# Kernel tuning notes

Hardware: AMD Instinct MI355X
Metric: run time of the kernel (lower is better)

Reference implementation:

```python
import jax, jax.numpy as jnp
import numpy as np

NUM_HEADS = 8
GROUPS = 32
EPS = 1e-5


def setup_inputs() -> dict:
    key = jax.random.key(0)
    k1, k2, k3 = jax.random.split(key, 3)
    B, C, H, W = 16, 512, 64, 64
    x = jax.random.normal(k1, (B, C, H, W), dtype=jnp.float32)
    scale = C ** -0.5  # keep qkv/proj outputs well-scaled
    return {
        "x": x,
        "norm_w": jnp.ones((C,), jnp.float32),
        "norm_b": jnp.zeros((C,), jnp.float32),
        "qkv_w": jax.random.normal(k2, (3 * C, C), dtype=jnp.float32) * scale,
        "qkv_b": jnp.zeros((3 * C,), jnp.float32),
        "proj_w": jax.random.normal(k3, (C, C), dtype=jnp.float32) * scale,
        "proj_b": jnp.zeros((C,), jnp.float32),
    }


def reference(x, norm_w, norm_b, qkv_w, qkv_b, proj_w, proj_b):
    B, C, H, W = x.shape
    N = H * W
    nh = NUM_HEADS
    hd = C // nh

    # GroupNorm(32, C)
    xg = x.reshape(B, GROUPS, C // GROUPS, N)
    mu = xg.mean(axis=(2, 3), keepdims=True)
    var = xg.var(axis=(2, 3), keepdims=True)
    h = ((xg - mu) * jax.lax.rsqrt(var + EPS)).reshape(B, C, N)
    h = h * norm_w[None, :, None] + norm_b[None, :, None]

    h = h.transpose(0, 2, 1)  # [B, N, C]
    qkv = (h @ qkv_w.T + qkv_b).reshape(B, N, 3, nh, hd)
    q, k, v = qkv[:, :, 0], qkv[:, :, 1], qkv[:, :, 2]  # each [B, N, nh, hd]

    # Faithful to source: attention over the HEAD axis at each position
    attn = jnp.einsum('bnhd,bngd->bnhg', q, k) * (hd ** -0.5)  # [B, N, nh, nh]
    attn = jax.nn.softmax(attn, axis=-1)
    o = jnp.einsum('bnhg,bngd->bnhd', attn, v).reshape(B, N, C)

    o = o @ proj_w.T + proj_b  # [B, N, C]
    return x + o.transpose(0, 2, 1).reshape(B, C, H, W)
```

## Files before the change

### kernel.cpp

```cpp
#include <hip/hip_runtime.h>

typedef __attribute__((ext_vector_type(8))) short short8v;
typedef __attribute__((ext_vector_type(4))) float float4v;
typedef unsigned short ushortT;

__device__ __forceinline__ unsigned short f2bf(float f) {
  union { float f; unsigned u; } a; a.f = f;
  unsigned r = a.u + 0x7fffu + ((a.u >> 16) & 1u);
  return (unsigned short)(r >> 16);
}
__device__ __forceinline__ float2 up2(unsigned u) {
  union { unsigned u; float f; } a, b;
  a.u = u << 16; b.u = u & 0xffff0000u;
  return make_float2(a.f, b.f);
}
__device__ __forceinline__ void gl_lds16(const void* g, void* l) {
  __builtin_amdgcn_global_load_lds(
      (const __attribute__((address_space(1))) void*)g,
      (__attribute__((address_space(3))) void*)l, 16, 0, 0);
}

#define WAITV4 asm volatile("s_waitcnt vmcnt(4)" ::: "memory")
#define WAITV0 asm volatile("s_waitcnt vmcnt(0)" ::: "memory")
#define BAR()  __builtin_amdgcn_s_barrier()
#define MFMA16(d, a, b) d = __builtin_amdgcn_mfma_f32_16x16x32_bf16(a, b, d, 0, 0, 0)

__global__ __launch_bounds__(256) void prep(const float* __restrict__ qkvw,
                                            const float* __restrict__ pw,
                                            const float* __restrict__ x,
                                            ushortT* __restrict__ wq_b,
                                            ushortT* __restrict__ wp_b,
                                            float2* __restrict__ stats) {
  int bid = blockIdx.x, tid = threadIdx.x;
  if (bid < 1024) {
    const float* src = (bid < 768) ? qkvw : pw;
    ushortT* dst     = (bid < 768) ? wq_b : wp_b;
    int base = (bid < 768) ? bid : (bid - 768);
    int i = (base * 256 + tid) * 4;
    float4 v = *(const float4*)(src + i);
    uint2 o;
    o.x = (unsigned)f2bf(v.x) | ((unsigned)f2bf(v.y) << 16);
    o.y = (unsigned)f2bf(v.z) | ((unsigned)f2bf(v.w) << 16);
    *(uint2*)(dst + i) = o;
    return;
  }
  int bg = bid - 1024;
  const float* base = x + (size_t)bg * 65536;
  float s = 0.f, s2 = 0.f;
  for (int i = tid; i < 16384; i += 256) {
    float4 v = *(const float4*)(base + (size_t)i * 4);
    s  += v.x + v.y + v.z + v.w;
    s2 += v.x * v.x + v.y * v.y + v.z * v.z + v.w * v.w;
  }
  #pragma unroll
  for (int off = 32; off > 0; off >>= 1) {
    s  += __shfl_down(s, off);
    s2 += __shfl_down(s2, off);
  }
  __shared__ float red[8];
  int w = tid >> 6, l = tid & 63;
  if (l == 0) { red[w] = s; red[w + 4] = s2; }
  __syncthreads();
  if (tid == 0) {
    float ts = red[0] + red[1] + red[2] + red[3];
    float t2 = red[4] + red[5] + red[6] + red[7];
    float mean = ts * (1.f / 65536.f);
    float var  = t2 * (1.f / 65536.f) - mean * mean;
    stats[bg] = make_float2(mean, rsqrtf(var + 1e-5f));
  }
}

__global__ __launch_bounds__(512) void norm_tr(const float* __restrict__ x,
                                               const float* __restrict__ nw,
                                               const float* __restrict__ nb,
                                               const float2* __restrict__ stats,
                                               ushortT* __restrict__ h) {
  __shared__ float t[64][65];
  int n0 = blockIdx.x * 64, c0 = blockIdx.y * 64, b = blockIdx.z;
  int tx = threadIdx.x, ty = threadIdx.y;
  #pragma unroll
  for (int j = ty; j < 64; j += 8) {
    int c = c0 + j;
    float2 ms = stats[b * 32 + (c >> 4)];
    float v = x[((size_t)b * 512 + c) * 4096 + n0 + tx];
    t[j][tx] = (v - ms.x) * ms.y * nw[c] + nb[c];
  }
  __syncthreads();
  #pragma unroll
  for (int j = ty; j < 64; j += 8) {
    int n = n0 + j;
    h[((size_t)b * 4096 + n) * 512 + c0 + tx] = f2bf(t[tx][j]);
  }
}

__device__ __forceinline__ void core256b(const ushortT* __restrict__ A,
                                         const ushortT* __restrict__ Bm,
                                         ushortT* lds, int m0, int n0,
                                         float4v (&acc)[8][4]) {
  char* ldsb = (char*)lds;
  const int tid = threadIdx.x;
  const int w = tid >> 6, l = tid & 63;
  const int wm = w >> 2, wn = w & 3;

  const int P0b = tid * 16, P1b = 8192 + tid * 16;
  const int r0 = P0b >> 7, r1 = P1b >> 7;
  const int s0 = (P0b & 127) ^ ((r0 & 7) << 4);
  const int s1 = (P1b & 127) ^ ((r1 & 7) << 4);
  const size_t g0 = (size_t)r0 * 512 + (s0 >> 1);
  const size_t g1 = (size_t)r1 * 512 + (s1 >> 1);
  auto stage = [&](const ushortT* mat, int rowbase, int kt, int bufb, int region) {
    const ushortT* gsrc = mat + (size_t)rowbase * 512 + kt * 64;
    char* dbase = ldsb + bufb + region;
    gl_lds16(gsrc + g0, dbase + P0b);
    gl_lds16(gsrc + g1, dbase + P1b);
  };

  const int colb = (l >> 4) * 16;
  const int cs0 = colb ^ ((l & 7) << 4);
  const int cs1 = (64 + colb) ^ ((l & 7) << 4);
  const int arow = wm * 16384 + (l & 15) * 128;
  const int brow = 32768 + wn * 8192 + (l & 15) * 128;

  short8v Af[4][2], Bf[4][2];

  #define RDA4(bb, MH)                                                  \
    { _Pragma("unroll")                                                 \
      for (int mm = 0; mm < 4; ++mm) {                                  \
        const char* p = ldsb + (bb) + arow + ((MH)*4 + mm) * 2048;      \
        Af[mm][0] = *(const short8v*)(p + cs0);                         \
        Af[mm][1] = *(const short8v*)(p + cs1);                         \
      } }
  #define RDB2(bb, N0)                                                  \
    { _Pragma("unroll")                                                 \
      for (int nn = 0; nn < 2; ++nn) {                                  \
        const char* p = ldsb + (bb) + brow + ((N0) + nn) * 2048;        \
        Bf[(N0)+nn][0] = *(const short8v*)(p + cs0);                    \
        Bf[(N0)+nn][1] = *(const short8v*)(p + cs1);                    \
      } }
  #define CLUSTER(MH, NP)                                               \
    { __builtin_amdgcn_s_setprio(1);                                    \
      _Pragma("unroll")                                                 \
      for (int mm = 0; mm < 4; ++mm) {                                  \
        _Pragma("unroll")                                               \
        for (int nn = 0; nn < 2; ++nn) {                                \
          MFMA16(acc[(MH)*4+mm][(NP)*2+nn], Af[mm][0], Bf[(NP)*2+nn][0]); \
          MFMA16(acc[(MH)*4+mm][(NP)*2+nn], Af[mm][1], Bf[(NP)*2+nn][1]); \
        } }                                                             \
      __builtin_amdgcn_s_setprio(0); }

  auto tile = [&](int bb, int t1, int t2, bool s1g, bool s2g, int vw) {
    RDB2(bb, 0); RDA4(bb, 0);
    if (s1g) stage(A, m0 + 128, t1, bb ^ 65536, 16384);
    BAR();
    CLUSTER(0, 0);
    BAR();
    RDB2(bb, 2);
    if (s1g) stage(Bm, n0 + 128, t1, bb ^ 65536, 49152);
    BAR();
    CLUSTER(0, 1);
    BAR();
    RDA4(bb, 1);
    if (s2g) stage(Bm, n0, t2, bb, 32768);
    BAR();
    CLUSTER(1, 1);
    BAR();
    if (s2g) stage(A, m0, t2, bb, 0);
    if (vw == 4)      { WAITV4; }
    else if (vw == 0) { WAITV0; }
    BAR();
    CLUSTER(1, 0);
    BAR();
  };

  stage(A,  m0,       0, 0, 0);
  stage(A,  m0 + 128, 0, 0, 16384);
  stage(Bm, n0,       0, 0, 32768);
  stage(Bm, n0 + 128, 0, 0, 49152);
  stage(Bm, n0,       1, 65536, 32768);
  stage(A,  m0,       1, 65536, 0);
  WAITV4;
  BAR();

  #pragma unroll 1
  for (int tp = 0; tp < 3; ++tp) {
    tile(0,     2 * tp + 1, 2 * tp + 2, true, true, 4);
    tile(65536, 2 * tp + 2, 2 * tp + 3, true, true, 4);
  }
  tile(0,     7, 8, true,  false, 0);
  tile(65536, 8, 9, false, false, -1);
  #undef RDA4
  #undef RDB2
  #undef CLUSTER
}

__device__ __forceinline__ void core128(const ushortT* __restrict__ A,
                                        const ushortT* __restrict__ Bm,
                                        ushortT* lds, int m0, int n0,
                                        float4v (&acc)[4][4]) {
  char* ldsb = (char*)lds;
  const int tid = threadIdx.x;
  const int w = tid >> 6, l = tid & 63;
  const int wm = w >> 1, wn = w & 1;

  const int r0 = tid >> 2, r1 = (256 + tid) >> 2;
  const int s0 = (tid & 3) ^ ((r0 >> 1) & 3);
  const int s1 = (tid & 3) ^ ((r1 >> 1) & 3);
  const size_t gA0 = (size_t)r0 * 512 + s0 * 8;
  const size_t gA1 = (size_t)r1 * 512 + s1 * 8;
  const int d0 = tid * 16, d1 = (256 + tid) * 16;

  const int cs = ((l >> 4) ^ (((l & 15) >> 1) & 3)) * 16;
  const int ab = wm * 4096 + (l & 15) * 64 + cs;
  const int bb = 8192 + wn * 4096 + (l & 15) * 64 + cs;

  const ushortT* pa = A + (size_t)m0 * 512;
  const ushortT* pb = Bm + (size_t)n0 * 512;

  #pragma unroll 1
  for (int kt = 0; kt < 16; ++kt) {
    if (kt) __syncthreads();
    gl_lds16(pa + gA0 + kt * 32, ldsb + d0);
    gl_lds16(pa + gA1 + kt * 32, ldsb + d1);
    gl_lds16(pb + gA0 + kt * 32, ldsb + 8192 + d0);
    gl_lds16(pb + gA1 + kt * 32, ldsb + 8192 + d1);
    __syncthreads();
    short8v Af[4], Bf[4];
    #pragma unroll
    for (int i = 0; i < 4; ++i) {
      Af[i] = *(const short8v*)(ldsb + ab + i * 1024);
      Bf[i] = *(const short8v*)(ldsb + bb + i * 1024);
    }
    #pragma unroll
    for (int mi = 0; mi < 4; ++mi)
      #pragma unroll
      for (int ni = 0; ni < 4; ++ni)
        MFMA16(acc[mi][ni], Af[mi], Bf[ni]);
  }
}

__global__ __launch_bounds__(512, 2) void gemm_qkv(const ushortT* __restrict__ h,
                                                   const ushortT* __restrict__ wq,
                                                   const float* __restrict__ bias,
                                                   ushortT* __restrict__ outq) {
  __shared__ ushortT lds[65536];
  int bid = blockIdx.x;
  int wg = (bid & 7) * 192 + (bid >> 3);
  int m0 = (wg / 6) * 256, n0 = (wg % 6) * 256;
  float4v acc[8][4] = {};
  core256b(h, wq, lds, m0, n0, acc);
  const int tid = threadIdx.x;
  const int w = tid >> 6, l = tid & 63;
  const int wm = w >> 2, wn = w & 3;
  __syncthreads();
  ushortT* es = lds + w * 1280;
  float bb[4];
  #pragma unroll
  for (int fn = 0; fn < 4; ++fn) bb[fn] = bias[n0 + wn * 64 + fn * 16 + (l & 15)];
  int r = l >> 2, g = l & 3;
  #pragma unroll
  for (int fm = 0; fm < 8; ++fm) {
    #pragma unroll
    for (int fn = 0; fn < 4; ++fn)
      #pragma unroll
      for (int j = 0; j < 4; ++j)
        es[((l >> 4) * 4 + j) * 72 + fn * 16 + (l & 15)] = f2bf(acc[fm][fn][j] + bb[fn]);
    uint4 v0 = *(const uint4*)(es + r * 72 + g * 16);
    uint4 v1 = *(const uint4*)(es + r * 72 + g * 16 + 8);
    size_t mrow = (size_t)m0 + wm * 128 + fm * 16 + r;
    uint4* dst = (uint4*)(outq + mrow * 1536 + n0 + wn * 64 + g * 16);
    dst[0] = v0; dst[1] = v1;
  }
}

__global__ __launch_bounds__(256) void attn_k(const ushortT* __restrict__ qkv,
                                              ushortT* __restrict__ o) {
  __shared__ ushortT kv[16 * 1544];
  const int tid = threadIdx.x;
  const int p0 = blockIdx.x * 16;

  #pragma unroll
  for (int j = 0; j < 12; ++j) {
    int c = j * 256 + tid;
    int row = c / 192, col = c % 192;
    gl_lds16(qkv + (size_t)(p0 + row) * 1536 + col * 8,
             (char*)kv + row * 3088 + col * 16);
  }
  __syncthreads();

  const int pos = tid >> 4, h = (tid >> 1) & 7, dh = tid & 1;
  const ushortT* rowp = kv + pos * 1544;

  unsigned qv[16];
  {
    const uint4* qs = (const uint4*)(rowp + h * 64 + dh * 32);
    #pragma unroll
    for (int i = 0; i < 4; ++i) {
      uint4 u = qs[i];
      qv[i*4+0] = u.x; qv[i*4+1] = u.y; qv[i*4+2] = u.z; qv[i*4+3] = u.w;
    }
  }
  float lg[8];
  #pragma unroll
  for (int g = 0; g < 8; ++g) {
    const uint4* ks = (const uint4*)(rowp + 512 + g * 64 + dh * 32);
    float s = 0.f;
    #pragma unroll
    for (int i = 0; i < 4; ++i) {
      uint4 u = ks[i];
      float2 k0 = up2(u.x), k1 = up2(u.y), k2 = up2(u.z), k3 = up2(u.w);
      float2 q0 = up2(qv[i*4+0]), q1 = up2(qv[i*4+1]);
      float2 q2 = up2(qv[i*4+2]), q3 = up2(qv[i*4+3]);
      s += q0.x*k0.x + q0.y*k0.y + q1.x*k1.x + q1.y*k1.y
         + q2.x*k2.x + q2.y*k2.y + q3.x*k3.x + q3.y*k3.y;
    }
    s += __shfl_xor(s, 1);
    lg[g] = s * 0.125f;
  }
  float mx = lg[0];
  #pragma unroll
  for (int g = 1; g < 8; ++g) mx = fmaxf(mx, lg[g]);
  float ssum = 0.f;
  #pragma unroll
  for (int g = 0; g < 8; ++g) { lg[g] = __expf(lg[g] - mx); ssum += lg[g]; }
  float inv = 1.f / ssum;
  #pragma unroll
  for (int g = 0; g < 8; ++g) lg[g] *= inv;

  float oa[32];
  #pragma unroll
  for (int i = 0; i < 32; ++i) oa[i] = 0.f;
  #pragma unroll
  for (int g = 0; g < 8; ++g) {
    const uint4* vs = (const uint4*)(rowp + 1024 + g * 64 + dh * 32);
    float wg = lg[g];
    #pragma unroll
    for (int i = 0; i < 4; ++i) {
      uint4 u = vs[i];
      float2 v0 = up2(u.x), v1 = up2(u.y), v2 = up2(u.z), v3 = up2(u.w);
      oa[i*8+0] += wg*v0.x; oa[i*8+1] += wg*v0.y;
      oa[i*8+2] += wg*v1.x; oa[i*8+3] += wg*v1.y;
      oa[i*8+4] += wg*v2.x; oa[i*8+5] += wg*v2.y;
      oa[i*8+6] += wg*v3.x; oa[i*8+7] += wg*v3.y;
    }
  }
  ushortT* dst = o + (size_t)(p0 + pos) * 512 + h * 64 + dh * 32;
  #pragma unroll
  for (int i = 0; i < 4; ++i) {
    uint4 w_;
    w_.x = (unsigned)f2bf(oa[i*8+0]) | ((unsigned)f2bf(oa[i*8+1]) << 16);
    w_.y = (unsigned)f2bf(oa[i*8+2]) | ((unsigned)f2bf(oa[i*8+3]) << 16);
    w_.z = (unsigned)f2bf(oa[i*8+4]) | ((unsigned)f2bf(oa[i*8+5]) << 16);
    w_.w = (unsigned)f2bf(oa[i*8+6]) | ((unsigned)f2bf(oa[i*8+7]) << 16);
    *(uint4*)(dst + i * 8) = w_;
  }
}

__global__ __launch_bounds__(256) void gemm_proj(const ushortT* __restrict__ o,
                                                 const ushortT* __restrict__ wp,
                                                 const float* __restrict__ bias,
                                                 const float* __restrict__ x,
                                                 float* __restrict__ out) {
  __shared__ ushortT lds[8192];
  int bid = blockIdx.x;
  int wg = (bid & 7) * 256 + (bid >> 3);
  int m0 = (wg >> 2) * 128, n0 = (wg & 3) * 128;
  float4v acc[4][4] = {};
  core128(o, wp, lds, m0, n0, acc);
  const int tid = threadIdx.x;
  const int w = tid >> 6, l = tid & 63;
  const int wm = w >> 1, wn = w & 1;
  __syncthreads();
  float* es = (float*)lds + w * 1024;
  int b = m0 >> 12;
  int c = n0 + wn * 64 + l;
  float bc = bias[c];
  const float* xrow = x + ((size_t)b * 512 + c) * 4096;
  float* orow = out + ((size_t)b * 512 + c) * 4096;
  int nb0 = (m0 & 4095) + wm * 64;
  #pragma unroll
  for (int fm = 0; fm < 4; ++fm) {
    #pragma unroll
    for (int fn = 0; fn < 4; ++fn)
      #pragma unroll
      for (int j = 0; j < 4; ++j)
        es[((l >> 4) * 4 + j) * 64 + fn * 16 + (l & 15)] = acc[fm][fn][j];
    int nb = nb0 + fm * 16;
    #pragma unroll
    for (int q4 = 0; q4 < 4; ++q4) {
      float4 xv = *(const float4*)(xrow + nb + q4 * 4);
      float4 ov;
      ov.x = xv.x + bc + es[(q4 * 4 + 0) * 64 + l];
      ov.y = xv.y + bc + es[(q4 * 4 + 1) * 64 + l];
      ov.z = xv.z + bc + es[(q4 * 4 + 2) * 64 + l];
      ov.w = xv.w + bc + es[(q4 * 4 + 3) * 64 + l];
      *(float4*)(orow + nb + q4 * 4) = ov;
    }
  }
}

extern "C" void kernel_launch(void* const* d_in, const int* in_sizes, int n_in,
                              void* d_out, int out_size, void* d_ws, size_t ws_size,
                              hipStream_t stream) {
  const float* x     = (const float*)d_in[0];
  const float* nw    = (const float*)d_in[1];
  const float* nb    = (const float*)d_in[2];
  const float* qkvw  = (const float*)d_in[3];
  const float* qkvb  = (const float*)d_in[4];
  const float* pw    = (const float*)d_in[5];
  const float* pb    = (const float*)d_in[6];
  float* out = (float*)d_out;
  char* ws = (char*)d_ws;

  const size_t OFF_WQ   = 4096;
  const size_t OFF_WP   = OFF_WQ + 1572864;
  const size_t OFF_H    = OFF_WP + 524288;
  const size_t OFF_QKV  = OFF_H + 67108864;

  float2* stats   = (float2*)ws;
  ushortT* wq_b   = (ushortT*)(ws + OFF_WQ);
  ushortT* wp_b   = (ushortT*)(ws + OFF_WP);
  ushortT* h      = (ushortT*)(ws + OFF_H);
  ushortT* qkv    = (ushortT*)(ws + OFF_QKV);

  prep<<<1536, 256, 0, stream>>>(qkvw, pw, x, wq_b, wp_b, stats);
  norm_tr<<<dim3(64, 8, 16), dim3(64, 8), 0, stream>>>(x, nw, nb, stats, h);
  gemm_qkv<<<1536, 512, 0, stream>>>(h, wq_b, qkvb, qkv);
  attn_k<<<4096, 256, 0, stream>>>(qkv, h);
  gemm_proj<<<2048, 256, 0, stream>>>(h, wp_b, pb, x, out);
}
```

Baseline: 353.4 us.

## Process two M-tiles per QKV GEMM block, prefetching the next tile's first K-slice

The QKV GEMM kernel is inlined and each workgroup now computes two consecutive 256x256 output tiles, so the grid is halved. While the last K-step of the first tile runs, the first K-slice of the second tile is staged into the idle LDS buffer. The epilogue staging area is moved to an LDS region that does not overlap the prefetched data. This aims to hide pipeline fill and epilogue latency between tiles. The cost is more complex control flow, fewer blocks for wave balancing, and more register pressure.

```diff
diff --git a/kernel.cpp b/kernel.cpp
--- a/kernel.cpp
+++ b/kernel.cpp
@@ -93,11 +93,17 @@
   }
 }
 
-__device__ __forceinline__ void core256b(const ushortT* __restrict__ A,
-                                         const ushortT* __restrict__ Bm,
-                                         ushortT* lds, int m0, int n0,
-                                         float4v (&acc)[8][4]) {
+__global__ __launch_bounds__(512, 2) void gemm_qkv(const ushortT* __restrict__ h,
+                                                   const ushortT* __restrict__ wq,
+                                                   const float* __restrict__ bias,
+                                                   ushortT* __restrict__ outq) {
+  __shared__ ushortT lds[65536];
   char* ldsb = (char*)lds;
+  int bid = blockIdx.x;
+  int wg = (bid & 7) * 96 + (bid >> 3);
+  const int m0s = (wg / 6) * 512;
+  const int n0  = (wg % 6) * 256;
+
   const int tid = threadIdx.x;
   const int w = tid >> 6, l = tid & 63;
   const int wm = w >> 2, wn = w & 3;
@@ -121,6 +127,7 @@
   const int arow = wm * 16384 + (l & 15) * 128;
   const int brow = 32768 + wn * 8192 + (l & 15) * 128;
 
+  float4v acc[8][4];
   short8v Af[4][2], Bf[4][2];
 
   #define RDA4(bb, MH)                                                  \
@@ -148,23 +155,23 @@
         } }                                                             \
       __builtin_amdgcn_s_setprio(0); }
 
-  auto tile = [&](int bb, int t1, int t2, bool s1g, bool s2g, int vw) {
+  auto tile = [&](int bb, int t1, int t2, bool s1g, bool s2g, int vw, int mc) {
     RDB2(bb, 0); RDA4(bb, 0);
-    if (s1g) stage(A, m0 + 128, t1, bb ^ 65536, 16384);
+    if (s1g) stage(h, mc + 128, t1, bb ^ 65536, 16384);
     BAR();
     CLUSTER(0, 0);
     BAR();
     RDB2(bb, 2);
-    if (s1g) stage(Bm, n0 + 128, t1, bb ^ 65536, 49152);
+    if (s1g) stage(wq, n0 + 128, t1, bb ^ 65536, 49152);
     BAR();
     CLUSTER(0, 1);
     BAR();
     RDA4(bb, 1);
-    if (s2g) stage(Bm, n0, t2, bb, 32768);
+    if (s2g) stage(wq, n0, t2, bb, 32768);
     BAR();
     CLUSTER(1, 1);
     BAR();
-    if (s2g) stage(A, m0, t2, bb, 0);
+    if (s2g) stage(h, mc, t2, bb, 0);
     if (vw == 4)      { WAITV4; }
     else if (vw == 0) { WAITV0; }
     BAR();
@@ -172,25 +179,168 @@
     BAR();
   };
 
-  stage(A,  m0,       0, 0, 0);
-  stage(A,  m0 + 128, 0, 0, 16384);
-  stage(Bm, n0,       0, 0, 32768);
-  stage(Bm, n0 + 128, 0, 0, 49152);
-  stage(Bm, n0,       1, 65536, 32768);
-  stage(A,  m0,       1, 65536, 0);
-  WAITV4;
-  BAR();
+  auto epilogue = [&](int mc) {
+    ushortT* es = (ushortT*)(ldsb + (w < 6 ? 81920 + w * 2560
+                                           : 114688 + (w - 6) * 2560));
+    float bb4[4];
+    #pragma unroll
+    for (int fn = 0; fn < 4; ++fn)
+      bb4[fn] = bias[n0 + wn * 64 + fn * 16 + (l & 15)];
+    int r = l >> 2, g = l & 3;
+    #pragma unroll
+    for (int fm = 0; fm < 8; ++fm) {
+      #pragma unroll
+      for (int fn = 0; fn < 4; ++fn)
+        #pragma unroll
+        for (int j = 0; j < 4; ++j)
+          es[((l >> 4) * 4 + j) * 72 + fn * 16 + (l & 15)] = f2bf(acc[fm][fn][j] + bb4[fn]);
+      uint4 v0 = *(const uint4*)(es + r * 72 + g * 16);
+      uint4 v1 = *(const uint4*)(es + r * 72 + g * 16 + 8);
+      size_t mrow = (size_t)mc + wm * 128 + fm * 16 + r;
+      uint4* dst = (uint4*)(outq + mrow * 1536 + n0 + wn * 64 + g * 16);
+      dst[0] = v0; dst[1] = v1;
+    }
+  };
 
   #pragma unroll 1
-  for (int tp = 0; tp < 3; ++tp) {
-    tile(0,     2 * tp + 1, 2 * tp + 2, true, true, 4);
-    tile(65536, 2 * tp + 2, 2 * tp + 3, true, true, 4);
-  }
-  tile(0,     7, 8, true,  false, 0);
-  tile(65536, 8, 9, false, false, -1);
+  for (int half = 0; half < 2; ++half) {
+    const int mc = m0s + half * 256;
+    #pragma unroll
+    for (int i = 0; i < 8; ++i)
+      #pragma unroll
+      for (int j = 0; j < 4; ++j)
+        acc[i][j] = (float4v){0.f, 0.f, 0.f, 0.f};
+
+    if (half == 0) {
+      stage(h,  mc,       0, 0, 0);
+      stage(h,  mc + 128, 0, 0, 16384);
+      stage(wq, n0,       0, 0, 32768);
+      stage(wq, n0 + 128, 0, 0, 49152);
+      stage(wq, n0,       1, 65536, 32768);
+      stage(h,  mc,       1, 65536, 0);
+      WAITV4;
+      BAR();
+    } else {
+      stage(wq, n0, 1, 65536, 32768);
+      stage(h,  mc, 1, 65536, 0);
+      BAR();
+    }
+
+    #pragma unroll 1
+    for (int tp = 0; tp < 3; ++tp) {
+      tile(0,     2 * tp + 1, 2 * tp + 2, true, true, 4, mc);
+      tile(65536, 2 * tp + 2, 2 * tp + 3, true, true, 4, mc);
+    }
+    tile(0, 7, 8, true, false, 0, mc);
+
+    if (half == 0) {
+      const int mc2 = mc + 256;
+      RDB2(65536, 0); RDA4(65536, 0);
+      stage(h, mc2, 0, 0, 0);
+      BAR(); CLUSTER(0, 0); BAR();
+      RDB2(65536, 2);
+      stage(h, mc2 + 128, 0, 0, 16384);
+      BAR(); CLUSTER(0, 1); BAR();
+      RDA4(65536, 1);
+      stage(wq, n0, 0, 0, 32768);
+      BAR(); CLUSTER(1, 1); BAR();
+      stage(wq, n0 + 128, 0, 0, 49152);
+      BAR(); CLUSTER(1, 0); BAR();
+    } else {
+      tile(65536, 8, 9, false, false, -1, mc);
+    }
+
+    __syncthreads();
+    epilogue(mc);
+    __syncthreads();
+    if (half == 0) { WAITV0; BAR(); }
+  }
   #undef RDA4
   #undef RDB2
   #undef CLUSTER
+}
+
+__global__ __launch_bounds__(256) void attn_k(const ushortT* __restrict__ qkv,
+                                              ushortT* __restrict__ o) {
+  __shared__ ushortT kv[16 * 1544];
+  const int tid = threadIdx.x;
+  const int p0 = blockIdx.x * 16;
+
+  #pragma unroll
+  for (int j = 0; j < 12; ++j) {
+    int c = j * 256 + tid;
+    int row = c / 192, col = c % 192;
+    gl_lds16(qkv + (size_t)(p0 + row) * 1536 + col * 8,
+             (char*)kv + row * 3088 + col * 16);
+  }
+  __syncthreads();
+
+  const int pos = tid >> 4, h = (tid >> 1) & 7, dh = tid & 1;
+  const ushortT* rowp = kv + pos * 1544;
+
+  unsigned qv[16];
+  {
+    const uint4* qs = (const uint4*)(rowp + h * 64 + dh * 32);
+    #pragma unroll
+    for (int i = 0; i < 4; ++i) {
+      uint4 u = qs[i];
+      qv[i*4+0] = u.x; qv[i*4+1] = u.y; qv[i*4+2] = u.z; qv[i*4+3] = u.w;
+    }
+  }
+  float lg[8];
+  #pragma unroll
+  for (int g = 0; g < 8; ++g) {
+    const uint4* ks = (const uint4*)(rowp + 512 + g * 64 + dh * 32);
+    float s = 0.f;
+    #pragma unroll
+    for (int i = 0; i < 4; ++i) {
+      uint4 u = ks[i];
+      float2 k0 = up2(u.x), k1 = up2(u.y), k2 = up2(u.z), k3 = up2(u.w);
+      float2 q0 = up2(qv[i*4+0]), q1 = up2(qv[i*4+1]);
+      float2 q2 = up2(qv[i*4+2]), q3 = up2(qv[i*4+3]);
+      s += q0.x*k0.x + q0.y*k0.y + q1.x*k1.x + q1.y*k1.y
+         + q2.x*k2.x + q2.y*k2.y + q3.x*k3.x + q3.y*k3.y;
+    }
+    s += __shfl_xor(s, 1);
+    lg[g] = s * 0.125f;
+  }
+  float mx = lg[0];
+  #pragma unroll
+  for (int g = 1; g < 8; ++g) mx = fmaxf(mx, lg[g]);
+  float ssum = 0.f;
+  #pragma unroll
+  for (int g = 0; g < 8; ++g) { lg[g] = __expf(lg[g] - mx); ssum += lg[g]; }
+  float inv = 1.f / ssum;
+  #pragma unroll
+  for (int g = 0; g < 8; ++g) lg[g] *= inv;
+
+  float oa[32];
+  #pragma unroll
+  for (int i = 0; i < 32; ++i) oa[i] = 0.f;
+  #pragma unroll
+  for (int g = 0; g < 8; ++g) {
+    const uint4* vs = (const uint4*)(rowp + 1024 + g * 64 + dh * 32);
+    float wg = lg[g];
+    #pragma unroll
+    for (int i = 0; i < 4; ++i) {
+      uint4 u = vs[i];
+      float2 v0 = up2(u.x), v1 = up2(u.y), v2 = up2(u.z), v3 = up2(u.w);
+      oa[i*8+0] += wg*v0.x; oa[i*8+1] += wg*v0.y;
+      oa[i*8+2] += wg*v1.x; oa[i*8+3] += wg*v1.y;
+      oa[i*8+4] += wg*v2.x; oa[i*8+5] += wg*v2.y;
+      oa[i*8+6] += wg*v3.x; oa[i*8+7] += wg*v3.y;
+    }
+  }
+  ushortT* dst = o + (size_t)(p0 + pos) * 512 + h * 64 + dh * 32;
+  #pragma unroll
+  for (int i = 0; i < 4; ++i) {
+    uint4 w_;
+    w_.x = (unsigned)f2bf(oa[i*8+0]) | ((unsigned)f2bf(oa[i*8+1]) << 16);
+    w_.y = (unsigned)f2bf(oa[i*8+2]) | ((unsigned)f2bf(oa[i*8+3]) << 16);
+    w_.z = (unsigned)f2bf(oa[i*8+4]) | ((unsigned)f2bf(oa[i*8+5]) << 16);
+    w_.w = (unsigned)f2bf(oa[i*8+6]) | ((unsigned)f2bf(oa[i*8+7]) << 16);
+    *(uint4*)(dst + i * 8) = w_;
+  }
 }
 
 __device__ __forceinline__ void core128(const ushortT* __restrict__ A,
@@ -235,123 +385,6 @@
       #pragma unroll
       for (int ni = 0; ni < 4; ++ni)
         MFMA16(acc[mi][ni], Af[mi], Bf[ni]);
-  }
-}
-
-__global__ __launch_bounds__(512, 2) void gemm_qkv(const ushortT* __restrict__ h,
-                                                   const ushortT* __restrict__ wq,
-                                                   const float* __restrict__ bias,
-                                                   ushortT* __restrict__ outq) {
-  __shared__ ushortT lds[65536];
-  int bid = blockIdx.x;
-  int wg = (bid & 7) * 192 + (bid >> 3);
-  int m0 = (wg / 6) * 256, n0 = (wg % 6) * 256;
-  float4v acc[8][4] = {};
-  core256b(h, wq, lds, m0, n0, acc);
-  const int tid = threadIdx.x;
-  const int w = tid >> 6, l = tid & 63;
-  const int wm = w >> 2, wn = w & 3;
-  __syncthreads();
-  ushortT* es = lds + w * 1280;
-  float bb[4];
-  #pragma unroll
-  for (int fn = 0; fn < 4; ++fn) bb[fn] = bias[n0 + wn * 64 + fn * 16 + (l & 15)];
-  int r = l >> 2, g = l & 3;
-  #pragma unroll
-  for (int fm = 0; fm < 8; ++fm) {
-    #pragma unroll
-    for (int fn = 0; fn < 4; ++fn)
-      #pragma unroll
-      for (int j = 0; j < 4; ++j)
-        es[((l >> 4) * 4 + j) * 72 + fn * 16 + (l & 15)] = f2bf(acc[fm][fn][j] + bb[fn]);
-    uint4 v0 = *(const uint4*)(es + r * 72 + g * 16);
-    uint4 v1 = *(const uint4*)(es + r * 72 + g * 16 + 8);
-    size_t mrow = (size_t)m0 + wm * 128 + fm * 16 + r;
-    uint4* dst = (uint4*)(outq + mrow * 1536 + n0 + wn * 64 + g * 16);
-    dst[0] = v0; dst[1] = v1;
-  }
-}
-
-__global__ __launch_bounds__(256) void attn_k(const ushortT* __restrict__ qkv,
-                                              ushortT* __restrict__ o) {
-  __shared__ ushortT kv[16 * 1544];
-  const int tid = threadIdx.x;
-  const int p0 = blockIdx.x * 16;
-
-  #pragma unroll
-  for (int j = 0; j < 12; ++j) {
-    int c = j * 256 + tid;
-    int row = c / 192, col = c % 192;
-    gl_lds16(qkv + (size_t)(p0 + row) * 1536 + col * 8,
-             (char*)kv + row * 3088 + col * 16);
-  }
-  __syncthreads();
-
-  const int pos = tid >> 4, h = (tid >> 1) & 7, dh = tid & 1;
-  const ushortT* rowp = kv + pos * 1544;
-
-  unsigned qv[16];
-  {
-    const uint4* qs = (const uint4*)(rowp + h * 64 + dh * 32);
-    #pragma unroll
-    for (int i = 0; i < 4; ++i) {
-      uint4 u = qs[i];
-      qv[i*4+0] = u.x; qv[i*4+1] = u.y; qv[i*4+2] = u.z; qv[i*4+3] = u.w;
-    }
-  }
-  float lg[8];
-  #pragma unroll
-  for (int g = 0; g < 8; ++g) {
-    const uint4* ks = (const uint4*)(rowp + 512 + g * 64 + dh * 32);
-    float s = 0.f;
-    #pragma unroll
-    for (int i = 0; i < 4; ++i) {
-      uint4 u = ks[i];
-      float2 k0 = up2(u.x), k1 = up2(u.y), k2 = up2(u.z), k3 = up2(u.w);
-      float2 q0 = up2(qv[i*4+0]), q1 = up2(qv[i*4+1]);
-      float2 q2 = up2(qv[i*4+2]), q3 = up2(qv[i*4+3]);
-      s += q0.x*k0.x + q0.y*k0.y + q1.x*k1.x + q1.y*k1.y
-         + q2.x*k2.x + q2.y*k2.y + q3.x*k3.x + q3.y*k3.y;
-    }
-    s += __shfl_xor(s, 1);
-    lg[g] = s * 0.125f;
-  }
-  float mx = lg[0];
-  #pragma unroll
-  for (int g = 1; g < 8; ++g) mx = fmaxf(mx, lg[g]);
-  float ssum = 0.f;
-  #pragma unroll
-  for (int g = 0; g < 8; ++g) { lg[g] = __expf(lg[g] - mx); ssum += lg[g]; }
-  float inv = 1.f / ssum;
-  #pragma unroll
-  for (int g = 0; g < 8; ++g) lg[g] *= inv;
-
-  float oa[32];
-  #pragma unroll
-  for (int i = 0; i < 32; ++i) oa[i] = 0.f;
-  #pragma unroll
-  for (int g = 0; g < 8; ++g) {
-    const uint4* vs = (const uint4*)(rowp + 1024 + g * 64 + dh * 32);
-    float wg = lg[g];
-    #pragma unroll
-    for (int i = 0; i < 4; ++i) {
-      uint4 u = vs[i];
-      float2 v0 = up2(u.x), v1 = up2(u.y), v2 = up2(u.z), v3 = up2(u.w);
-      oa[i*8+0] += wg*v0.x; oa[i*8+1] += wg*v0.y;
-      oa[i*8+2] += wg*v1.x; oa[i*8+3] += wg*v1.y;
-      oa[i*8+4] += wg*v2.x; oa[i*8+5] += wg*v2.y;
-      oa[i*8+6] += wg*v3.x; oa[i*8+7] += wg*v3.y;
-    }
-  }
-  ushortT* dst = o + (size_t)(p0 + pos) * 512 + h * 64 + dh * 32;
-  #pragma unroll
-  for (int i = 0; i < 4; ++i) {
-    uint4 w_;
-    w_.x = (unsigned)f2bf(oa[i*8+0]) | ((unsigned)f2bf(oa[i*8+1]) << 16);
-    w_.y = (unsigned)f2bf(oa[i*8+2]) | ((unsigned)f2bf(oa[i*8+3]) << 16);
-    w_.z = (unsigned)f2bf(oa[i*8+4]) | ((unsigned)f2bf(oa[i*8+5]) << 16);
-    w_.w = (unsigned)f2bf(oa[i*8+6]) | ((unsigned)f2bf(oa[i*8+7]) << 16);
-    *(uint4*)(dst + i * 8) = w_;
   }
 }
 
@@ -424,7 +457,7 @@
 
   prep<<<1536, 256, 0, stream>>>(qkvw, pw, x, wq_b, wp_b, stats);
   norm_tr<<<dim3(64, 8, 16), dim3(64, 8), 0, stream>>>(x, nw, nb, stats, h);
-  gemm_qkv<<<1536, 512, 0, stream>>>(h, wq_b, qkvb, qkv);
+  gemm_qkv<<<768, 512, 0, stream>>>(h, wq_b, qkvb, qkv);
   attn_k<<<4096, 256, 0, stream>>>(qkv, h);
   gemm_proj<<<2048, 256, 0, stream>>>(h, wp_b, pb, x, out);
 }
```

After: 536.6 us. 51.8% more time.
